# Kernel tuning notes

Hardware: AMD Instinct MI355X
Metric: run time of the kernel (lower is better)

## Reference

```python
import jax, jax.numpy as jnp
import numpy as np

L, S, D, H, DL, V, B = 8, 1024, 768, 12, 64, 512, 8
NB, NM = 32, 64  # big_bird neighbours, global memory columns


def _bigbird_mask():
    i = np.arange(S)[:, None]
    j = np.arange(S)[None, :]
    m = ((np.abs(i - j) <= NB) | (j < NM)) & (j <= i)  # window + global cols, then tril
    return jnp.asarray(m)[None, None]  # [1,1,S,S]


def _ln(x, g, b):
    mu = x.mean(-1, keepdims=True)
    var = ((x - mu) ** 2).mean(-1, keepdims=True)
    return (x - mu) / jnp.sqrt(var + 1e-5) * g + b


def setup_inputs() -> dict:
    key = jax.random.key(0)
    ks = jax.random.split(key, 16)
    s = 0.02
    d = {
        'x': jax.random.randint(ks[0], (B, S), 0, V),
        'targets': jax.random.randint(ks[1], (B, S), 0, V),
        'wte': jax.random.normal(ks[2], (V, D), jnp.float32) * s,
        'pos': jnp.zeros((1, S, D), jnp.float32),
        'ln1_g': jnp.ones((L, D)), 'ln1_b': jnp.zeros((L, D)),
        'wq': jax.random.normal(ks[3], (L, D, D)) * s, 'bq': jnp.zeros((L, D)),
        'wk': jax.random.normal(ks[4], (L, D, D)) * s, 'bk': jnp.zeros((L, D)),
        'wv': jax.random.normal(ks[5], (L, D, D)) * s, 'bv': jnp.zeros((L, D)),
        'ln2_g': jnp.ones((L, D)), 'ln2_b': jnp.zeros((L, D)),
        'w1': jax.random.normal(ks[6], (L, D, 4 * D)) * s, 'b1': jnp.zeros((L, 4 * D)),
        'w2': jax.random.normal(ks[7], (L, 4 * D, D)) * s, 'b2': jnp.zeros((L, D)),
        'lnf_g': jnp.ones((D,)), 'lnf_b': jnp.zeros((D,)),
        'w_out': jax.random.normal(ks[8], (D, V)) * s,
    }
    return d


def _forward(x, targets, wte, pos, ln1_g, ln1_b, wq, bq, wk, bk, wv, bv,
             ln2_g, ln2_b, w1, b1, w2, b2, lnf_g, lnf_b, w_out):
    mask = _bigbird_mask()
    h = wte[x] + pos  # [B,S,D]
    scale = DL ** -0.5
    neg_inf = jnp.array(float('-inf'), h.dtype)
    for l in range(L):
        a = _ln(h, ln1_g[l], ln1_b[l])
        q = (a @ wq[l] + bq[l]).reshape(B, S, H, DL).transpose(0, 2, 1, 3)
        k = (a @ wk[l] + bk[l]).reshape(B, S, H, DL).transpose(0, 2, 1, 3)
        v = (a @ wv[l] + bv[l]).reshape(B, S, H, DL).transpose(0, 2, 1, 3)
        att = jnp.einsum('bhqd,bhkd->bhqk', q, k) * scale
        att = jnp.where(mask, att, neg_inf)
        att = jax.nn.softmax(att, axis=-1)
        z = jnp.einsum('bhqk,bhkd->bhqd', att, v)
        z = z.transpose(0, 2, 1, 3).reshape(B, S, D)
        h = h + z  # note: W_0 is defined in the torch module but never applied
        m = _ln(h, ln2_g[l], ln2_b[l])
        h = h + jax.nn.gelu(m @ w1[l] + b1[l], approximate=False) @ w2[l] + b2[l]
    h = _ln(h, lnf_g, lnf_b)
    pred = h @ w_out  # [B,S,V]
    logp = jax.nn.log_softmax(pred.reshape(B * S, V), axis=-1)
    loss = -jnp.take_along_axis(logp, targets.reshape(-1, 1), axis=1).mean()
    return pred, loss


def reference(x, targets, wte, pos, ln1_g, ln1_b, wq, bq, wk, bk, wv, bv,
              ln2_g, ln2_b, w1, b1, w2, b2, lnf_g, lnf_b, w_out):
    return _forward(x, targets, wte, pos, ln1_g, ln1_b, wq, bq, wk, bk, wv, bv,
                    ln2_g, ln2_b, w1, b1, w2, b2, lnf_g, lnf_b, w_out)
```

## Files before the change

kernel.cpp:

```cpp
#include <hip/hip_runtime.h>
#include <hip/hip_bf16.h>

#define DEV __device__ __forceinline__

typedef __attribute__((ext_vector_type(8))) short short8;
typedef __attribute__((ext_vector_type(4))) float f32x4;

DEV unsigned short f2bf(float f){
  unsigned int u = __builtin_bit_cast(unsigned int, f);
  u += 0x7FFFu + ((u >> 16) & 1u);
  return (unsigned short)(u >> 16);
}

DEV void gld_lds16(const void* g, void* l){
  __builtin_amdgcn_global_load_lds((const __attribute__((address_space(1))) void*)g,
                                   (__attribute__((address_space(3))) void*)l, 16, 0, 0);
}

__global__ void k_embed(const int* __restrict__ x, const float* __restrict__ wte,
                        const float* __restrict__ pos, float* __restrict__ h){
  int i = blockIdx.x * 256 + threadIdx.x;
  int row = i / 768, d = i - row * 768;
  int s = row & 1023;
  h[i] = wte[x[row] * 768 + d] + pos[s * 768 + d];
}

__global__ void k_ln(const float* __restrict__ src, const float* __restrict__ g,
                     const float* __restrict__ b, unsigned short* __restrict__ out){
  int row = blockIdx.x, t = threadIdx.x;
  const float* p = src + (size_t)row * 768;
  float v0 = p[t], v1 = p[t + 256], v2 = p[t + 512];
  float s = v0 + v1 + v2;
  float sq = v0 * v0 + v1 * v1 + v2 * v2;
  #pragma unroll
  for(int m = 32; m >= 1; m >>= 1){ s += __shfl_xor(s, m); sq += __shfl_xor(sq, m); }
  __shared__ float red[8];
  int w = t >> 6;
  if((t & 63) == 0){ red[w] = s; red[4 + w] = sq; }
  __syncthreads();
  float S  = red[0] + red[1] + red[2] + red[3];
  float SQ = red[4] + red[5] + red[6] + red[7];
  float mu  = S * (1.0f / 768.0f);
  float var = SQ * (1.0f / 768.0f) - mu * mu;
  float inv = rsqrtf(var + 1e-5f);
  unsigned short* o = out + (size_t)row * 768;
  o[t]       = f2bf((v0 - mu) * inv * g[t]       + b[t]);
  o[t + 256] = f2bf((v1 - mu) * inv * g[t + 256] + b[t + 256]);
  o[t + 512] = f2bf((v2 - mu) * inv * g[t + 512] + b[t + 512]);
}

DEV void tr_tile(float (*tl)[33], const float* __restrict__ src, unsigned short* __restrict__ dst,
                 int R, int C, int tx, int ty, int tid){
  int lx = tid & 31, ly = tid >> 5;
  int r0 = ty * 32, c0 = tx * 32;
  #pragma unroll
  for(int i = 0; i < 4; i++) tl[ly + 8*i][lx] = src[(size_t)(r0 + ly + 8*i) * C + (c0 + lx)];
  __syncthreads();
  #pragma unroll
  for(int i = 0; i < 4; i++) dst[(size_t)(c0 + ly + 8*i) * R + (r0 + lx)] = f2bf(tl[lx][ly + 8*i]);
}

__global__ void k_convert_layer(const float* __restrict__ wq, const float* __restrict__ wk,
                                const float* __restrict__ wv, const float* __restrict__ w1,
                                const float* __restrict__ w2, const float* __restrict__ bq,
                                const float* __restrict__ bk, const float* __restrict__ bv,
                                unsigned short* __restrict__ wqkv_t, unsigned short* __restrict__ w1_t,
                                unsigned short* __restrict__ w2_t, float* __restrict__ qkv_bias){
  __shared__ float tl[32][33];
  int bid = blockIdx.x, tid = threadIdx.x;
  if(bid < 1728){
    int which = bid / 576, t = bid - which * 576;
    const float* src = which == 0 ? wq : which == 1 ? wk : wv;
    tr_tile(tl, src, wqkv_t + (size_t)which * 589824, 768, 768, t % 24, t / 24, tid);
  } else if(bid < 1728 + 2304){
    int t = bid - 1728;
    tr_tile(tl, w1, w1_t, 768, 3072, t % 96, t / 96, tid);
  } else if(bid < 1728 + 4608){
    int t = bid - 4032;
    tr_tile(tl, w2, w2_t, 3072, 768, t % 24, t / 24, tid);
  } else {
    for(int i = tid; i < 768; i += 256){
      qkv_bias[i] = bq[i]; qkv_bias[768 + i] = bk[i]; qkv_bias[1536 + i] = bv[i];
    }
  }
}

__global__ void k_transpose(const float* __restrict__ src, unsigned short* __restrict__ dst,
                            int R, int C){
  __shared__ float tl[32][33];
  int nx = C / 32;
  tr_tile(tl, src, dst, R, C, blockIdx.x % nx, blockIdx.x / nx, threadIdx.x);
}

template<int EPI>
__global__ __launch_bounds__(256)
void k_gemm(const unsigned short* __restrict__ A, const unsigned short* __restrict__ Bt,
            const float* __restrict__ bias, int K,
            float* __restrict__ fout, unsigned short* __restrict__ o0,
            unsigned short* __restrict__ o1, unsigned short* __restrict__ o2){
  __shared__ unsigned short As[128 * 64];
  __shared__ unsigned short Bs[128 * 64];
  int tid = threadIdx.x, w = tid >> 6, lane = tid & 63;
  int nbx = gridDim.x;
  int bid = blockIdx.y * nbx + blockIdx.x;
  int cpx = (nbx * gridDim.y) >> 3;
  int sid = (bid & 7) * cpx + (bid >> 3);
  int bm = sid / nbx, bn = sid - bm * nbx;
  int N = nbx * 128;
  int wr = w >> 1, wc = w & 1;
  f32x4 acc[4][4] = {};
  int rowA[4], colA[4];
  #pragma unroll
  for(int i = 0; i < 4; i++){
    int o = ((i * 4 + w) << 10) + (lane << 4);
    int r = o >> 7;
    int ch = (o >> 4) & 7;
    rowA[i] = r;
    colA[i] = ((ch ^ (r & 7)) << 3);
  }
  const size_t aBase = (size_t)bm * 128;
  const size_t bBase = (size_t)bn * 128;
  for(int kt = 0; kt < K; kt += 64){
    #pragma unroll
    for(int i = 0; i < 4; i++){
      gld_lds16(A  + (aBase + rowA[i]) * K + kt + colA[i], (char*)As + ((i * 4 + w) << 10));
      gld_lds16(Bt + (bBase + rowA[i]) * K + kt + colA[i], (char*)Bs + ((i * 4 + w) << 10));
    }
    __syncthreads();
    #pragma unroll
    for(int s = 0; s < 2; s++){
      short8 af[4], bfr[4];
      #pragma unroll
      for(int m = 0; m < 4; m++){
        int r = wr * 64 + m * 16 + (lane & 15);
        int ch = s * 4 + (lane >> 4);
        af[m] = *(const short8*)(As + r * 64 + ((ch ^ (r & 7)) << 3));
      }
      #pragma unroll
      for(int n = 0; n < 4; n++){
        int r = wc * 64 + n * 16 + (lane & 15);
        int ch = s * 4 + (lane >> 4);
        bfr[n] = *(const short8*)(Bs + r * 64 + ((ch ^ (r & 7)) << 3));
      }
      #pragma unroll
      for(int m = 0; m < 4; m++)
        #pragma unroll
        for(int n = 0; n < 4; n++)
          acc[m][n] = __builtin_amdgcn_mfma_f32_16x16x32_bf16(af[m], bfr[n], acc[m][n], 0, 0, 0);
    }
    __syncthreads();
  }
  int r0 = bm * 128 + wr * 64 + ((lane >> 4) << 2);
  int c0 = bn * 128 + wc * 64 + (lane & 15);
  if(EPI == 0){
    unsigned short* dstn[4];
    float bv4[4];
    #pragma unroll
    for(int n = 0; n < 4; n++){
      int col = c0 + n * 16;
      bv4[n] = bias[col];
      int which = col / 768, cc = col - which * 768;
      int hd = cc >> 6, dl = cc & 63;
      unsigned short* dst = which == 0 ? o0 : which == 1 ? o1 : o2;
      dstn[n] = dst + (size_t)hd * 65536 + dl;
    }
    #pragma unroll
    for(int m = 0; m < 4; m++){
      #pragma unroll
      for(int j = 0; j < 4; j++){
        int row = r0 + m * 16 + j;
        int bb = row >> 10, sp = row & 1023;
        size_t ro = ((size_t)bb * 12288 + sp) * 64;
        #pragma unroll
        for(int n = 0; n < 4; n++)
          dstn[n][ro] = f2bf(acc[m][n][j] + bv4[n]);
      }
    }
  } else {
    float bv4[4];
    #pragma unroll
    for(int n = 0; n < 4; n++) bv4[n] = (EPI == 3) ? 0.0f : bias[c0 + n * 16];
    #pragma unroll
    for(int m = 0; m < 4; m++){
      #pragma unroll
      for(int j = 0; j < 4; j++){
        int row = r0 + m * 16 + j;
        #pragma unroll
        for(int n = 0; n < 4; n++){
          int col = c0 + n * 16;
          float v = acc[m][n][j] + bv4[n];
          if(EPI == 1){
            float t = v * (1.5957691f + 0.07135481f * v * v);
            float gl = v * __builtin_amdgcn_rcpf(1.0f + __expf(-t));
            o0[(size_t)row * N + col] = f2bf(gl);
          } else if(EPI == 2){
            fout[(size_t)row * 768 + col] += v;
          } else {
            fout[(size_t)row * 512 + col] = v;
          }
        }
      }
    }
  }
}

__global__ __launch_bounds__(256)
void k_attn(const unsigned short* __restrict__ qg, const unsigned short* __restrict__ kg,
            const unsigned short* __restrict__ vg, float* __restrict__ h){
  __shared__ unsigned short Vt[64 * 256];
  __shared__ unsigned short Ps[4][32 * 128];
  int qb = blockIdx.x, bh = blockIdx.y;
  int tid = threadIdx.x, w = tid >> 6, lane = tid & 63;
  int b = bh / 12, hd = bh - b * 12;
  int wbase = qb * 128 - 32;
  const unsigned short* vb = vg + (size_t)bh * 1024 * 64;
  for(int u = tid; u < 224 * 8; u += 256){
    int slot = u >> 3, c8 = u & 7;
    int j = slot < 64 ? slot : wbase + (slot - 64);
    if(j < 0) j = 0;
    short8 vv = *(const short8*)(vb + (size_t)j * 64 + c8 * 8);
    #pragma unroll
    for(int e = 0; e < 8; e++){
      int d = c8 * 8 + e;
      Vt[d * 256 + (((slot >> 3) ^ (d & 7)) << 3) + (slot & 7)] = (unsigned short)vv[e];
    }
  }
  __syncthreads();
  int i0 = qb * 128 + 32 * w;
  const unsigned short* qrow = qg + (size_t)bh * 1024 * 64;
  const unsigned short* krow = kg + (size_t)bh * 1024 * 64;
  short8 qf[2][2];
  #pragma unroll
  for(int m = 0; m < 2; m++)
    #pragma unroll
    for(int s = 0; s < 2; s++)
      qf[m][s] = *(const short8*)(qrow + (size_t)(i0 + m * 16 + (lane & 15)) * 64 + s * 32 + ((lane >> 4) << 3));
  f32x4 sacc[2][8] = {};
  #pragma unroll
  for(int n = 0; n < 8; n++){
    int jk = (n < 4) ? (n * 16 + (lane & 15))
                     : (wbase + 32 * w + (n - 4) * 16 + (lane & 15));
    int jc = jk < 0 ? 0 : jk;
    const unsigned short* kr = krow + (size_t)jc * 64 + ((lane >> 4) << 3);
    short8 k0 = *(const short8*)(kr);
    short8 k1 = *(const short8*)(kr + 32);
    #pragma unroll
    for(int m = 0; m < 2; m++){
      sacc[m][n] = __builtin_amdgcn_mfma_f32_16x16x32_bf16(qf[m][0], k0, sacc[m][n], 0, 0, 0);
      sacc[m][n] = __builtin_amdgcn_mfma_f32_16x16x32_bf16(qf[m][1], k1, sacc[m][n], 0, 0, 0);
    }
  }
  #pragma unroll
  for(int m = 0; m < 2; m++)
    #pragma unroll
    for(int n = 0; n < 8; n++){
      int s_ = n * 16 + (lane & 15);
      int jkey = (n < 4) ? s_ : (wbase + 32 * w + (s_ - 64));
      #pragma unroll
      for(int j = 0; j < 4; j++){
        int qi = i0 + m * 16 + ((lane >> 4) << 2) + j;
        bool ok = (n < 4) ? (jkey <= qi)
                          : (jkey >= 64 && jkey <= qi && (qi - jkey) <= 32);
        sacc[m][n][j] = ok ? sacc[m][n][j] * 0.125f : -1e30f;
      }
    }
  float rsum[2][4];
  #pragma unroll
  for(int m = 0; m < 2; m++)
    #pragma unroll
    for(int j = 0; j < 4; j++){
      float mx = sacc[m][0][j];
      #pragma unroll
      for(int n = 1; n < 8; n++) mx = fmaxf(mx, sacc[m][n][j]);
      mx = fmaxf(mx, __shfl_xor(mx, 1)); mx = fmaxf(mx, __shfl_xor(mx, 2));
      mx = fmaxf(mx, __shfl_xor(mx, 4)); mx = fmaxf(mx, __shfl_xor(mx, 8));
      float sm = 0.f;
      #pragma unroll
      for(int n = 0; n < 8; n++){
        float e = expf(sacc[m][n][j] - mx);
        sacc[m][n][j] = e;
        sm += e;
      }
      sm += __shfl_xor(sm, 1); sm += __shfl_xor(sm, 2);
      sm += __shfl_xor(sm, 4); sm += __shfl_xor(sm, 8);
      rsum[m][j] = sm;
    }
  unsigned short* Pw = Ps[w];
  #pragma unroll
  for(int m = 0; m < 2; m++)
    #pragma unroll
    for(int n = 0; n < 8; n++){
      int s_ = n * 16 + (lane & 15);
      #pragma unroll
      for(int j = 0; j < 4; j++){
        int ql = m * 16 + ((lane >> 4) << 2) + j;
        Pw[ql * 128 + (((s_ >> 3) ^ (ql & 7)) << 3) + (s_ & 7)] = f2bf(sacc[m][n][j]);
      }
    }
  f32x4 oacc[2][4] = {};
  #pragma unroll
  for(int s = 0; s < 4; s++){
    short8 pa[2];
    #pragma unroll
    for(int m = 0; m < 2; m++){
      int ql = m * 16 + (lane & 15);
      int ch = s * 4 + (lane >> 4);
      pa[m] = *(const short8*)(Pw + ql * 128 + ((ch ^ (ql & 7)) << 3));
    }
    int kk = s * 32 + ((lane >> 4) << 3);
    int slot0 = kk < 64 ? kk : 64 + 32 * w + (kk - 64);
    #pragma unroll
    for(int n = 0; n < 4; n++){
      int d = n * 16 + (lane & 15);
      short8 vv = *(const short8*)(Vt + d * 256 + (((slot0 >> 3) ^ (d & 7)) << 3));
      #pragma unroll
      for(int m = 0; m < 2; m++)
        oacc[m][n] = __builtin_amdgcn_mfma_f32_16x16x32_bf16(pa[m], vv, oacc[m][n], 0, 0, 0);
    }
  }
  #pragma unroll
  for(int m = 0; m < 2; m++)
    #pragma unroll
    for(int j = 0; j < 4; j++){
      int ql = m * 16 + ((lane >> 4) << 2) + j;
      float inv = 1.0f / rsum[m][j];
      size_t base = ((size_t)(b * 1024 + i0 + ql)) * 768 + hd * 64;
      #pragma unroll
      for(int n = 0; n < 4; n++){
        int d = n * 16 + (lane & 15);
        h[base + d] += oacc[m][n][j] * inv;
      }
    }
}

__global__ void k_rowloss(const float* __restrict__ pred, const int* __restrict__ tgt,
                          float* __restrict__ rowloss){
  int row = blockIdx.x * 4 + (threadIdx.x >> 6);
  int lane = threadIdx.x & 63;
  const float* p = pred + (size_t)row * 512 + lane * 8;
  float v[8];
  #pragma unroll
  for(int i = 0; i < 8; i++) v[i] = p[i];
  float mx = v[0];
  #pragma unroll
  for(int i = 1; i < 8; i++) mx = fmaxf(mx, v[i]);
  #pragma unroll
  for(int m = 1; m < 64; m <<= 1) mx = fmaxf(mx, __shfl_xor(mx, m));
  float se = 0.f;
  #pragma unroll
  for(int i = 0; i < 8; i++) se += expf(v[i] - mx);
  #pragma unroll
  for(int m = 1; m < 64; m <<= 1) se += __shfl_xor(se, m);
  int t = tgt[row];
  float pt = 0.f;
  int base = lane * 8;
  #pragma unroll
  for(int i = 0; i < 8; i++) pt = (t == base + i) ? v[i] : pt;
  #pragma unroll
  for(int m = 1; m < 64; m <<= 1) pt += __shfl_xor(pt, m);
  if(lane == 0) rowloss[row] = -(pt - mx - logf(se));
}

__global__ void k_lossfinal(const float* __restrict__ rowloss, float* __restrict__ out){
  int tid = threadIdx.x;
  float s = 0.f;
  for(int i = tid; i < 8192; i += 256) s += rowloss[i];
  #pragma unroll
  for(int m = 32; m >= 1; m >>= 1) s += __shfl_xor(s, m);
  __shared__ float red[4];
  if((tid & 63) == 0) red[tid >> 6] = s;
  __syncthreads();
  if(tid == 0) out[0] = (red[0] + red[1] + red[2] + red[3]) * (1.0f / 8192.0f);
}

extern "C" void kernel_launch(void* const* d_in, const int* in_sizes, int n_in,
                              void* d_out, int out_size, void* d_ws, size_t ws_size,
                              hipStream_t stream){
  const int*   x       = (const int*)d_in[0];
  const int*   targets = (const int*)d_in[1];
  const float* wte     = (const float*)d_in[2];
  const float* pos     = (const float*)d_in[3];
  const float* ln1_g   = (const float*)d_in[4];
  const float* ln1_b   = (const float*)d_in[5];
  const float* wq      = (const float*)d_in[6];
  const float* bq      = (const float*)d_in[7];
  const float* wk      = (const float*)d_in[8];
  const float* bk      = (const float*)d_in[9];
  const float* wv      = (const float*)d_in[10];
  const float* bv      = (const float*)d_in[11];
  const float* ln2_g   = (const float*)d_in[12];
  const float* ln2_b   = (const float*)d_in[13];
  const float* w1      = (const float*)d_in[14];
  const float* b1      = (const float*)d_in[15];
  const float* w2      = (const float*)d_in[16];
  const float* b2      = (const float*)d_in[17];
  const float* lnf_g   = (const float*)d_in[18];
  const float* lnf_b   = (const float*)d_in[19];
  const float* w_out   = (const float*)d_in[20];
  float* out = (float*)d_out;

  char* ws = (char*)d_ws;
  float*          h      = (float*)ws;
  unsigned short* a_bf   = (unsigned short*)(ws + 25165824);
  char*           big    = ws + 37748736;
  unsigned short* qbf    = (unsigned short*)big;
  unsigned short* kbf    = (unsigned short*)(big + 12582912);
  unsigned short* vbf    = (unsigned short*)(big + 25165824);
  unsigned short* tbf    = (unsigned short*)big;
  char*           wb     = ws + 88080384;
  unsigned short* wqkv_t = (unsigned short*)wb;
  unsigned short* w1_t   = (unsigned short*)(wb + 3538944);
  unsigned short* w2_t   = (unsigned short*)(wb + 8257536);
  float*          qkvb   = (float*)(ws + 101056512);
  float*          rowls  = (float*)(ws + 101065728);

  k_embed<<<24576, 256, 0, stream>>>(x, wte, pos, h);
  for(int l = 0; l < 8; l++){
    k_convert_layer<<<6337, 256, 0, stream>>>(
        wq + (size_t)l * 589824, wk + (size_t)l * 589824, wv + (size_t)l * 589824,
        w1 + (size_t)l * 2359296, w2 + (size_t)l * 2359296,
        bq + l * 768, bk + l * 768, bv + l * 768, wqkv_t, w1_t, w2_t, qkvb);
    k_ln<<<8192, 256, 0, stream>>>(h, ln1_g + l * 768, ln1_b + l * 768, a_bf);
    k_gemm<0><<<dim3(18, 64), 256, 0, stream>>>(a_bf, wqkv_t, qkvb, 768, nullptr, qbf, kbf, vbf);
    k_attn<<<dim3(8, 96), 256, 0, stream>>>(qbf, kbf, vbf, h);
    k_ln<<<8192, 256, 0, stream>>>(h, ln2_g + l * 768, ln2_b + l * 768, a_bf);
    k_gemm<1><<<dim3(24, 64), 256, 0, stream>>>(a_bf, w1_t, b1 + l * 3072, 768, nullptr, tbf, nullptr, nullptr);
    k_gemm<2><<<dim3(6, 64), 256, 0, stream>>>(tbf, w2_t, b2 + l * 768, 3072, h, nullptr, nullptr, nullptr);
  }
  k_ln<<<8192, 256, 0, stream>>>(h, lnf_g, lnf_b, a_bf);
  k_transpose<<<384, 256, 0, stream>>>(w_out, wqkv_t, 768, 512);
  k_gemm<3><<<dim3(4, 64), 256, 0, stream>>>(a_bf, wqkv_t, nullptr, 768, out, nullptr, nullptr, nullptr);
  k_rowloss<<<2048, 256, 0, stream>>>(out, targets, rowls);
  k_lossfinal<<<1, 256, 0, stream>>>(rowls, out + 4194304);
}
```

Measured before the change: 1.712 ms.

## Batch all-layer weight conversion upfront and use narrower GEMM tiles for small-N GEMMs

When the workspace is large enough, all eight layers' weights are transposed and converted to bf16 in one wide launch before the layer loop, replacing eight per-layer conversion launches. The GEMM gains a tile-width template parameter, and the W2 and output-projection GEMMs switch to 64-column tiles so their grids have more blocks for the small N. The W_out transpose moves to the start. The aim is to cut launch and serialisation overhead and to underfill the GPU less on narrow GEMMs. The cost is more workspace and lower per-block reuse of the A tile.

```diff
diff --git a/kernel.cpp b/kernel.cpp
--- a/kernel.cpp
+++ b/kernel.cpp
@@ -60,27 +60,37 @@
   for(int i = 0; i < 4; i++) dst[(size_t)(c0 + ly + 8*i) * R + (r0 + lx)] = f2bf(tl[lx][ly + 8*i]);
 }
 
-__global__ void k_convert_layer(const float* __restrict__ wq, const float* __restrict__ wk,
-                                const float* __restrict__ wv, const float* __restrict__ w1,
-                                const float* __restrict__ w2, const float* __restrict__ bq,
-                                const float* __restrict__ bk, const float* __restrict__ bv,
-                                unsigned short* __restrict__ wqkv_t, unsigned short* __restrict__ w1_t,
-                                unsigned short* __restrict__ w2_t, float* __restrict__ qkv_bias){
+__global__ void k_convert_all(const float* __restrict__ wq, const float* __restrict__ wk,
+                              const float* __restrict__ wv, const float* __restrict__ w1,
+                              const float* __restrict__ w2, const float* __restrict__ bq,
+                              const float* __restrict__ bk, const float* __restrict__ bv,
+                              unsigned short* __restrict__ wall, float* __restrict__ qkvb,
+                              int l0){
   __shared__ float tl[32][33];
+  int l = l0 + blockIdx.y, slot = blockIdx.y;
   int bid = blockIdx.x, tid = threadIdx.x;
+  unsigned short* wqkv_t = wall + (size_t)slot * 6488064;
+  unsigned short* w1_t   = wqkv_t + 1769472;
+  unsigned short* w2_t   = w1_t + 2359296;
+  float* qb = qkvb + slot * 2304;
+  const float* wq_l = wq + (size_t)l * 589824;
+  const float* wk_l = wk + (size_t)l * 589824;
+  const float* wv_l = wv + (size_t)l * 589824;
+  const float* w1_l = w1 + (size_t)l * 2359296;
+  const float* w2_l = w2 + (size_t)l * 2359296;
   if(bid < 1728){
     int which = bid / 576, t = bid - which * 576;
-    const float* src = which == 0 ? wq : which == 1 ? wk : wv;
+    const float* src = which == 0 ? wq_l : which == 1 ? wk_l : wv_l;
     tr_tile(tl, src, wqkv_t + (size_t)which * 589824, 768, 768, t % 24, t / 24, tid);
   } else if(bid < 1728 + 2304){
     int t = bid - 1728;
-    tr_tile(tl, w1, w1_t, 768, 3072, t % 96, t / 96, tid);
+    tr_tile(tl, w1_l, w1_t, 768, 3072, t % 96, t / 96, tid);
   } else if(bid < 1728 + 4608){
     int t = bid - 4032;
-    tr_tile(tl, w2, w2_t, 3072, 768, t % 24, t / 24, tid);
+    tr_tile(tl, w2_l, w2_t, 3072, 768, t % 24, t / 24, tid);
   } else {
     for(int i = tid; i < 768; i += 256){
-      qkv_bias[i] = bq[i]; qkv_bias[768 + i] = bk[i]; qkv_bias[1536 + i] = bv[i];
+      qb[i] = bq[l * 768 + i]; qb[768 + i] = bk[l * 768 + i]; qb[1536 + i] = bv[l * 768 + i];
     }
   }
 }
@@ -92,7 +102,7 @@
   tr_tile(tl, src, dst, R, C, blockIdx.x % nx, blockIdx.x / nx, threadIdx.x);
 }
 
-template<int EPI>
+template<int EPI, int NB>
 __global__ __launch_bounds__(256)
 void k_gemm(const unsigned short* __restrict__ A, const unsigned short* __restrict__ Bt,
             const float* __restrict__ bias, int K,
@@ -106,9 +116,9 @@
   int cpx = (nbx * gridDim.y) >> 3;
   int sid = (bid & 7) * cpx + (bid >> 3);
   int bm = sid / nbx, bn = sid - bm * nbx;
-  int N = nbx * 128;
+  int N = nbx * NB * 32;
   int wr = w >> 1, wc = w & 1;
-  f32x4 acc[4][4] = {};
+  f32x4 acc[4][NB] = {};
   int rowA[4], colA[4];
   #pragma unroll
   for(int i = 0; i < 4; i++){
@@ -119,17 +129,18 @@
     colA[i] = ((ch ^ (r & 7)) << 3);
   }
   const size_t aBase = (size_t)bm * 128;
-  const size_t bBase = (size_t)bn * 128;
+  const size_t bBase = (size_t)bn * (NB * 32);
   for(int kt = 0; kt < K; kt += 64){
     #pragma unroll
-    for(int i = 0; i < 4; i++){
-      gld_lds16(A  + (aBase + rowA[i]) * K + kt + colA[i], (char*)As + ((i * 4 + w) << 10));
+    for(int i = 0; i < 4; i++)
+      gld_lds16(A + (aBase + rowA[i]) * K + kt + colA[i], (char*)As + ((i * 4 + w) << 10));
+    #pragma unroll
+    for(int i = 0; i < NB; i++)
       gld_lds16(Bt + (bBase + rowA[i]) * K + kt + colA[i], (char*)Bs + ((i * 4 + w) << 10));
-    }
     __syncthreads();
     #pragma unroll
     for(int s = 0; s < 2; s++){
-      short8 af[4], bfr[4];
+      short8 af[4], bfr[NB];
       #pragma unroll
       for(int m = 0; m < 4; m++){
         int r = wr * 64 + m * 16 + (lane & 15);
@@ -137,28 +148,28 @@
         af[m] = *(const short8*)(As + r * 64 + ((ch ^ (r & 7)) << 3));
       }
       #pragma unroll
-      for(int n = 0; n < 4; n++){
-        int r = wc * 64 + n * 16 + (lane & 15);
+      for(int n = 0; n < NB; n++){
+        int r = wc * (NB * 16) + n * 16 + (lane & 15);
         int ch = s * 4 + (lane >> 4);
         bfr[n] = *(const short8*)(Bs + r * 64 + ((ch ^ (r & 7)) << 3));
       }
       #pragma unroll
       for(int m = 0; m < 4; m++)
         #pragma unroll
-        for(int n = 0; n < 4; n++)
+        for(int n = 0; n < NB; n++)
           acc[m][n] = __builtin_amdgcn_mfma_f32_16x16x32_bf16(af[m], bfr[n], acc[m][n], 0, 0, 0);
     }
     __syncthreads();
   }
   int r0 = bm * 128 + wr * 64 + ((lane >> 4) << 2);
-  int c0 = bn * 128 + wc * 64 + (lane & 15);
+  int c0 = bn * (NB * 32) + wc * (NB * 16) + (lane & 15);
   if(EPI == 0){
-    unsigned short* dstn[4];
-    float bv4[4];
-    #pragma unroll
-    for(int n = 0; n < 4; n++){
+    unsigned short* dstn[NB];
+    float bvn[NB];
+    #pragma unroll
+    for(int n = 0; n < NB; n++){
       int col = c0 + n * 16;
-      bv4[n] = bias[col];
+      bvn[n] = bias[col];
       int which = col / 768, cc = col - which * 768;
       int hd = cc >> 6, dl = cc & 63;
       unsigned short* dst = which == 0 ? o0 : which == 1 ? o1 : o2;
@@ -172,23 +183,23 @@
         int bb = row >> 10, sp = row & 1023;
         size_t ro = ((size_t)bb * 12288 + sp) * 64;
         #pragma unroll
-        for(int n = 0; n < 4; n++)
-          dstn[n][ro] = f2bf(acc[m][n][j] + bv4[n]);
+        for(int n = 0; n < NB; n++)
+          dstn[n][ro] = f2bf(acc[m][n][j] + bvn[n]);
       }
     }
   } else {
-    float bv4[4];
-    #pragma unroll
-    for(int n = 0; n < 4; n++) bv4[n] = (EPI == 3) ? 0.0f : bias[c0 + n * 16];
+    float bvn[NB];
+    #pragma unroll
+    for(int n = 0; n < NB; n++) bvn[n] = (EPI == 3) ? 0.0f : bias[c0 + n * 16];
     #pragma unroll
     for(int m = 0; m < 4; m++){
       #pragma unroll
       for(int j = 0; j < 4; j++){
         int row = r0 + m * 16 + j;
         #pragma unroll
-        for(int n = 0; n < 4; n++){
+        for(int n = 0; n < NB; n++){
           int col = c0 + n * 16;
-          float v = acc[m][n][j] + bv4[n];
+          float v = acc[m][n][j] + bvn[n];
           if(EPI == 1){
             float t = v * (1.5957691f + 0.07135481f * v * v);
             float gl = v * __builtin_amdgcn_rcpf(1.0f + __expf(-t));
@@ -407,29 +418,36 @@
   unsigned short* kbf    = (unsigned short*)(big + 12582912);
   unsigned short* vbf    = (unsigned short*)(big + 25165824);
   unsigned short* tbf    = (unsigned short*)big;
-  char*           wb     = ws + 88080384;
-  unsigned short* wqkv_t = (unsigned short*)wb;
-  unsigned short* w1_t   = (unsigned short*)(wb + 3538944);
-  unsigned short* w2_t   = (unsigned short*)(wb + 8257536);
-  float*          qkvb   = (float*)(ws + 101056512);
-  float*          rowls  = (float*)(ws + 101065728);
-
+  bool mega = ws_size >= 192782336ull;
+  unsigned short* wall   = (unsigned short*)(ws + 88080384);
+  size_t wend = 88080384ull + (mega ? 103809024ull : 12976128ull);
+  unsigned short* wout_t = (unsigned short*)(ws + wend);
+  float*          qkvb   = (float*)(ws + wend + 786432);
+  float*          rowls  = (float*)(ws + wend + 786432 + (mega ? 73728 : 9216));
+
+  if(mega)
+    k_convert_all<<<dim3(6337, 8), 256, 0, stream>>>(wq, wk, wv, w1, w2, bq, bk, bv,
+                                                     wall, qkvb, 0);
+  k_transpose<<<384, 256, 0, stream>>>(w_out, wout_t, 768, 512);
   k_embed<<<24576, 256, 0, stream>>>(x, wte, pos, h);
   for(int l = 0; l < 8; l++){
-    k_convert_layer<<<6337, 256, 0, stream>>>(
-        wq + (size_t)l * 589824, wk + (size_t)l * 589824, wv + (size_t)l * 589824,
-        w1 + (size_t)l * 2359296, w2 + (size_t)l * 2359296,
-        bq + l * 768, bk + l * 768, bv + l * 768, wqkv_t, w1_t, w2_t, qkvb);
+    if(!mega)
+      k_convert_all<<<dim3(6337, 1), 256, 0, stream>>>(wq, wk, wv, w1, w2, bq, bk, bv,
+                                                       wall, qkvb, l);
+    int slot = mega ? l : 0;
+    unsigned short* wqkv_l = wall + (size_t)slot * 6488064;
+    unsigned short* w1_l   = wqkv_l + 1769472;
+    unsigned short* w2_l   = w1_l + 2359296;
+    float*          qkvb_l = qkvb + slot * 2304;
     k_ln<<<8192, 256, 0, stream>>>(h, ln1_g + l * 768, ln1_b + l * 768, a_bf);
-    k_gemm<0><<<dim3(18, 64), 256, 0, stream>>>(a_bf, wqkv_t, qkvb, 768, nullptr, qbf, kbf, vbf);
+    k_gemm<0,4><<<dim3(18, 64), 256, 0, stream>>>(a_bf, wqkv_l, qkvb_l, 768, nullptr, qbf, kbf, vbf);
     k_attn<<<dim3(8, 96), 256, 0, stream>>>(qbf, kbf, vbf, h);
     k_ln<<<8192, 256, 0, stream>>>(h, ln2_g + l * 768, ln2_b + l * 768, a_bf);
-    k_gemm<1><<<dim3(24, 64), 256, 0, stream>>>(a_bf, w1_t, b1 + l * 3072, 768, nullptr, tbf, nullptr, nullptr);
-    k_gemm<2><<<dim3(6, 64), 256, 0, stream>>>(tbf, w2_t, b2 + l * 768, 3072, h, nullptr, nullptr, nullptr);
+    k_gemm<1,4><<<dim3(24, 64), 256, 0, stream>>>(a_bf, w1_l, b1 + l * 3072, 768, nullptr, tbf, nullptr, nullptr);
+    k_gemm<2,2><<<dim3(12, 64), 256, 0, stream>>>(tbf, w2_l, b2 + l * 768, 3072, h, nullptr, nullptr, nullptr);
   }
   k_ln<<<8192, 256, 0, stream>>>(h, lnf_g, lnf_b, a_bf);
-  k_transpose<<<384, 256, 0, stream>>>(w_out, wqkv_t, 768, 512);
-  k_gemm<3><<<dim3(4, 64), 256, 0, stream>>>(a_bf, wqkv_t, nullptr, 768, out, nullptr, nullptr, nullptr);
+  k_gemm<3,2><<<dim3(8, 64), 256, 0, stream>>>(a_bf, wout_t, nullptr, 768, out, nullptr, nullptr, nullptr);
   k_rowloss<<<2048, 256, 0, stream>>>(out, targets, rowls);
   k_lossfinal<<<1, 256, 0, stream>>>(rowls, out + 4194304);
 }
```

Measured after the change: 1.619 ms. -5.4%, faster.
